# Kernel tuning notes

Measured on AMD Instinct MI355X. Metric: run time of the kernel, lower is better.

## Reference

```python
import jax, jax.numpy as jnp
import numpy as np

B, C, H, W, K = 4, 32, 64, 64, 64
BH, BW = 2, 2  # block_size
RF_THRESH = 0.05  # gaussian support threshold (lattice kernels are ~0 outside RF)


def _gaussian_lattice(key, n_kernels, h, w):
    """Build Gaussian receptive-field kernels like lattice.gaussian_kernel_lattice:
    rfs[k,i,j] = exp(-((i-mu_y)^2 + (j-mu_x)^2) / (2*sigma^2)), thresholded to
    zero outside the RF so each kernel has compact support."""
    k1, k2 = jax.random.split(key)
    mu = jax.random.uniform(k1, (n_kernels, 2), minval=8.0, maxval=h - 8.0)
    sigma = jax.random.uniform(k2, (n_kernels, 1), minval=4.0, maxval=7.0)
    yy = jnp.arange(h, dtype=jnp.float32)[:, None]
    xx = jnp.arange(w, dtype=jnp.float32)[None, :]
    d2 = (yy[None] - mu[:, 0, None, None]) ** 2 + (xx[None] - mu[:, 1, None, None]) ** 2
    g = jnp.exp(-d2 / (2.0 * sigma[:, :, None] ** 2))  # (K, h, w)
    return jnp.where(g > RF_THRESH, g, 0.0).astype(jnp.float32)


def setup_inputs() -> dict:
    key = jax.random.key(0)
    ku, kr = jax.random.split(key)
    u = jax.random.normal(ku, (B, C, H, W), dtype=jnp.float32)
    rfs = _gaussian_lattice(kr, K, H, W)
    return {"u": u, "rfs": rfs}


def reference(u, rfs):
    """RF_Pool.__call__ with pool_type='prob', block_size=(2,2): returns p_mean.

    For each receptive field k, the kernel is elementwise-multiplied with u and
    a probabilistic max-pool (Lee et al.) with an 'off' state is computed over
    the RF support:  h_mean_k = exp(u*rf_k) / (1 + sum_{RF_k} exp(u*rf_k)).
    Detection probabilities are accumulated over RFs, then pooling-unit means
    p_mean are taken as the block-wise max over block_size blocks."""
    dt = u.dtype
    mask = rfs > 0  # (K, H, W) RF supports
    neg = jnp.asarray(-1e30, dt)
    # kernel-weighted pre-activations per RF: (B, C, K, H, W)
    v = u[:, :, None, :, :] * rfs[None, None]
    vm = jnp.where(mask[None, None], v, neg)
    # stable normalization including the off-state exp(0)=1
    m = jnp.maximum(jnp.max(vm, axis=(-2, -1), keepdims=True), 0.0)
    e = jnp.where(mask[None, None], jnp.exp(v - m), 0.0)
    denom = jnp.exp(-m) + jnp.sum(e, axis=(-2, -1), keepdims=True)
    h_mean = jnp.sum(e / denom, axis=2)  # (B, C, H, W) sum over RFs
    # block-wise pooling to p_mean: (B, C, H//BH, W//BW)
    p_mean = h_mean.reshape(B, C, H // BH, BH, W // BW, BW).max(axis=(3, 5))
    return p_mean
```

## Files before the change

### kernel.cpp

```cpp
#include <hip/hip_runtime.h>
#include <hip/hip_bf16.h>

#define BB 4
#define CC 32
#define HH 64
#define WW 64
#define KK 64
#define PIX (HH * WW)
#define NBC (BB * CC)


__global__ __launch_bounds__(256) void rf_phase1(
        const float* __restrict__ u,
        const float* __restrict__ rfs,
        float* __restrict__ inv) {
    const int bc = blockIdx.x >> 4;
    const int kg = blockIdx.x & 15;
    const int t  = threadIdx.x;
    const int w  = t >> 6;
    const int l  = t & 63;

    __shared__ float su[PIX];
    {
        const float4* u4  = (const float4*)(u + (size_t)bc * PIX);
        float4*       su4 = (float4*)su;
        #pragma unroll
        for (int i = 0; i < 4; ++i) su4[t + 256 * i] = u4[t + 256 * i];
    }
    __syncthreads();

    const int k = kg * 4 + w;
    const float4* r4  = (const float4*)(rfs + (size_t)k * PIX);
    const float4* su4 = (const float4*)su;

    float s = 0.f;
    #pragma unroll
    for (int i = 0; i < 16; ++i) {
        const float4 rv = r4[64 * i + l];
        const float4 uv = su4[64 * i + l];
        const float ex = __expf(uv.x * rv.x);
        const float ey = __expf(uv.y * rv.y);
        const float ez = __expf(uv.z * rv.z);
        const float ew = __expf(uv.w * rv.w);
        s += (rv.x > 0.f) ? ex : 0.f;
        s += (rv.y > 0.f) ? ey : 0.f;
        s += (rv.z > 0.f) ? ez : 0.f;
        s += (rv.w > 0.f) ? ew : 0.f;
    }
    #pragma unroll
    for (int off = 32; off > 0; off >>= 1)
        s += __shfl_xor(s, off, 64);

    if (l == 0) inv[bc * KK + k] = 1.f / (1.f + s);
}

__global__ __launch_bounds__(256) void rf_phase2(
        const float* __restrict__ u,
        const float* __restrict__ rfs,
        const float* __restrict__ inv,
        float* __restrict__ out) {
    const int bc = blockIdx.x >> 3;
    const int rp = (blockIdx.x & 7) * 4 + (threadIdx.x >> 6);
    const int l  = threadIdx.x & 63;

    const int pbase = rp * 128 + l;
    const float u0 = u[(size_t)bc * PIX + pbase];
    const float u1 = u[(size_t)bc * PIX + pbase + 64];
    const float* __restrict__ invp = inv + bc * KK;
    const float* __restrict__ rfp  = rfs + pbase;

    float h0 = 0.f, h1 = 0.f;
    #pragma unroll 8
    for (int k = 0; k < KK; ++k) {
        const float r0 = rfp[(size_t)k * PIX];
        const float r1 = rfp[(size_t)k * PIX + 64];
        const float fi = invp[k];
        const float e0 = __expf(u0 * r0);
        const float e1 = __expf(u1 * r1);
        h0 += (r0 > 0.f) ? e0 * fi : 0.f;
        h1 += (r1 > 0.f) ? e1 * fi : 0.f;
    }

    const float v = fmaxf(h0, h1);
    const float o = fmaxf(v, __shfl_xor(v, 1, 64));
    if ((l & 1) == 0)
        out[(size_t)bc * (HH / 2) * (WW / 2) + rp * 32 + (l >> 1)] = o;
}

extern "C" void kernel_launch(void* const* d_in, const int* in_sizes, int n_in,
                              void* d_out, int out_size, void* d_ws, size_t ws_size,
                              hipStream_t stream) {
    const float* u   = (const float*)d_in[0];
    const float* rfs = (const float*)d_in[1];
    float* out       = (float*)d_out;
    float* inv       = (float*)d_ws;

    rf_phase1<<<NBC * 16, 256, 0, stream>>>(u, rfs, inv);
    rf_phase2<<<NBC * 8, 256, 0, stream>>>(u, rfs, inv, out);
}
```

Before: 73.92 us.

## Skip work outside each receptive field's bounding box via precomputed bboxes

Adds a kernel that computes the row/column bounding box of each RF's nonzero support. The normalization pass and the accumulation pass then only load and exponentiate pixels inside each RF's box, instead of scanning the full 64x64 grid for every (bc,k). Phase1 drops its shared-memory staging of u, and phase2 caches inv and bboxes in shared memory. It adds a third launch and divergent per-lane branches, but the bboxes are derived from the inputs on every call, so correctness holds for any rfs.

```diff
diff --git a/kernel.cpp b/kernel.cpp
--- a/kernel.cpp
+++ b/kernel.cpp
@@ -10,81 +10,124 @@
 #define NBC (BB * CC)
 
 
+__global__ __launch_bounds__(256) void rf_bbox(
+        const float* __restrict__ rfs, int4* __restrict__ bbox) {
+    const int k = blockIdx.x;
+    const int t = threadIdx.x;
+    const int l = t & 63;
+
+    int minr = HH, maxr = -1, minc = WW, maxc = -1;
+    const float4* r4 = (const float4*)(rfs + (size_t)k * PIX);
+    #pragma unroll
+    for (int i = 0; i < 4; ++i) {
+        const float4 v = r4[t + 256 * i];
+        const int px = 4 * (t + 256 * i);
+        const int r = px >> 6, cbase = px & 63;
+        const float vv[4] = {v.x, v.y, v.z, v.w};
+        #pragma unroll
+        for (int j = 0; j < 4; ++j) {
+            if (vv[j] > 0.f) {
+                minr = min(minr, r);       maxr = max(maxr, r);
+                minc = min(minc, cbase + j); maxc = max(maxc, cbase + j);
+            }
+        }
+    }
+    #pragma unroll
+    for (int off = 32; off > 0; off >>= 1) {
+        minr = min(minr, __shfl_xor(minr, off, 64));
+        maxr = max(maxr, __shfl_xor(maxr, off, 64));
+        minc = min(minc, __shfl_xor(minc, off, 64));
+        maxc = max(maxc, __shfl_xor(maxc, off, 64));
+    }
+    __shared__ int sb[4];
+    if (t == 0) { sb[0] = HH; sb[1] = -1; sb[2] = WW; sb[3] = -1; }
+    __syncthreads();
+    if (l == 0) {
+        atomicMin(&sb[0], minr); atomicMax(&sb[1], maxr);
+        atomicMin(&sb[2], minc); atomicMax(&sb[3], maxc);
+    }
+    __syncthreads();
+    if (t == 0) bbox[k] = make_int4(sb[0], sb[1], sb[2], sb[3]);
+}
+
 __global__ __launch_bounds__(256) void rf_phase1(
         const float* __restrict__ u,
         const float* __restrict__ rfs,
+        const int4* __restrict__ bbox,
         float* __restrict__ inv) {
-    const int bc = blockIdx.x >> 4;
-    const int kg = blockIdx.x & 15;
-    const int t  = threadIdx.x;
-    const int w  = t >> 6;
-    const int l  = t & 63;
+    const int w   = threadIdx.x >> 6;
+    const int l   = threadIdx.x & 63;
+    const int idx = blockIdx.x * 4 + w;
+    const int bc  = idx >> 6;
+    const int k   = idx & 63;
 
-    __shared__ float su[PIX];
-    {
-        const float4* u4  = (const float4*)(u + (size_t)bc * PIX);
-        float4*       su4 = (float4*)su;
-        #pragma unroll
-        for (int i = 0; i < 4; ++i) su4[t + 256 * i] = u4[t + 256 * i];
-    }
-    __syncthreads();
+    const int4 bb = bbox[k];
+    const int colbase = (l & 15) * 4;
+    const bool colact = (colbase + 3 >= bb.z) && (colbase <= bb.w);
 
-    const int k = kg * 4 + w;
-    const float4* r4  = (const float4*)(rfs + (size_t)k * PIX);
-    const float4* su4 = (const float4*)su;
+    const float* rp = rfs + (size_t)k * PIX;
+    const float* up = u + (size_t)bc * PIX;
 
     float s = 0.f;
-    #pragma unroll
-    for (int i = 0; i < 16; ++i) {
-        const float4 rv = r4[64 * i + l];
-        const float4 uv = su4[64 * i + l];
-        const float ex = __expf(uv.x * rv.x);
-        const float ey = __expf(uv.y * rv.y);
-        const float ez = __expf(uv.z * rv.z);
-        const float ew = __expf(uv.w * rv.w);
-        s += (rv.x > 0.f) ? ex : 0.f;
-        s += (rv.y > 0.f) ? ey : 0.f;
-        s += (rv.z > 0.f) ? ez : 0.f;
-        s += (rv.w > 0.f) ? ew : 0.f;
+    for (int r = bb.x + (l >> 4); r <= bb.y; r += 4) {
+        if (colact) {
+            const float4 rv = *(const float4*)(rp + r * WW + colbase);
+            const float4 uv = *(const float4*)(up + r * WW + colbase);
+            s += (rv.x > 0.f) ? __expf(uv.x * rv.x) : 0.f;
+            s += (rv.y > 0.f) ? __expf(uv.y * rv.y) : 0.f;
+            s += (rv.z > 0.f) ? __expf(uv.z * rv.z) : 0.f;
+            s += (rv.w > 0.f) ? __expf(uv.w * rv.w) : 0.f;
+        }
     }
     #pragma unroll
     for (int off = 32; off > 0; off >>= 1)
         s += __shfl_xor(s, off, 64);
-
     if (l == 0) inv[bc * KK + k] = 1.f / (1.f + s);
 }
 
 __global__ __launch_bounds__(256) void rf_phase2(
         const float* __restrict__ u,
         const float* __restrict__ rfs,
+        const int4* __restrict__ bbox,
         const float* __restrict__ inv,
         float* __restrict__ out) {
-    const int bc = blockIdx.x >> 3;
-    const int rp = (blockIdx.x & 7) * 4 + (threadIdx.x >> 6);
-    const int l  = threadIdx.x & 63;
+    const int bc    = blockIdx.x >> 3;
+    const int chunk = blockIdx.x & 7;
+    const int t     = threadIdx.x;
+    const int w     = t >> 6;
+    const int l     = t & 63;
+    const int R0    = chunk * 8 + 2 * w;
 
-    const int pbase = rp * 128 + l;
-    const float u0 = u[(size_t)bc * PIX + pbase];
-    const float u1 = u[(size_t)bc * PIX + pbase + 64];
-    const float* __restrict__ invp = inv + bc * KK;
-    const float* __restrict__ rfp  = rfs + pbase;
+    __shared__ float sinv[KK];
+    __shared__ int4  sbb[KK];
+    if (t < KK) { sinv[t] = inv[bc * KK + t]; sbb[t] = bbox[t]; }
+
+    const float u0 = u[(size_t)bc * PIX + R0 * WW + l];
+    const float u1 = u[(size_t)bc * PIX + (R0 + 1) * WW + l];
+    __syncthreads();
 
     float h0 = 0.f, h1 = 0.f;
-    #pragma unroll 8
+    #pragma unroll 4
     for (int k = 0; k < KK; ++k) {
-        const float r0 = rfp[(size_t)k * PIX];
-        const float r1 = rfp[(size_t)k * PIX + 64];
-        const float fi = invp[k];
-        const float e0 = __expf(u0 * r0);
-        const float e1 = __expf(u1 * r1);
-        h0 += (r0 > 0.f) ? e0 * fi : 0.f;
-        h1 += (r1 > 0.f) ? e1 * fi : 0.f;
+        const int4 bb = sbb[k];
+        if (bb.y < R0 || bb.x > R0 + 1) continue;
+        const float fi = sinv[k];
+        const bool colact = (l >= bb.z) && (l <= bb.w);
+        const float* rp = rfs + (size_t)k * PIX + R0 * WW + l;
+        if (colact && R0 >= bb.x && R0 <= bb.y) {
+            const float rv = rp[0];
+            h0 += (rv > 0.f) ? __expf(u0 * rv) * fi : 0.f;
+        }
+        if (colact && R0 + 1 >= bb.x && R0 + 1 <= bb.y) {
+            const float rv = rp[WW];
+            h1 += (rv > 0.f) ? __expf(u1 * rv) * fi : 0.f;
+        }
     }
 
     const float v = fmaxf(h0, h1);
     const float o = fmaxf(v, __shfl_xor(v, 1, 64));
     if ((l & 1) == 0)
-        out[(size_t)bc * (HH / 2) * (WW / 2) + rp * 32 + (l >> 1)] = o;
+        out[(size_t)bc * (HH / 2) * (WW / 2) + (chunk * 4 + w) * 32 + (l >> 1)] = o;
 }
 
 extern "C" void kernel_launch(void* const* d_in, const int* in_sizes, int n_in,
@@ -93,8 +136,10 @@
     const float* u   = (const float*)d_in[0];
     const float* rfs = (const float*)d_in[1];
     float* out       = (float*)d_out;
-    float* inv       = (float*)d_ws;
+    int4* bbox       = (int4*)d_ws;
+    float* inv       = (float*)((char*)d_ws + KK * sizeof(int4));
 
-    rf_phase1<<<NBC * 16, 256, 0, stream>>>(u, rfs, inv);
-    rf_phase2<<<NBC * 8, 256, 0, stream>>>(u, rfs, inv, out);
+    rf_bbox  <<<KK, 256, 0, stream>>>(rfs, bbox);
+    rf_phase1<<<NBC * KK / 4, 256, 0, stream>>>(u, rfs, bbox, inv);
+    rf_phase2<<<NBC * 8, 256, 0, stream>>>(u, rfs, bbox, inv, out);
 }
```

Result: slower. 88.39 us (+19.6%).

## Fuse normaliser and accumulation kernels into one block-per-image-half kernel

Applied to the files above, without the earlier changes.

Merges the two kernels into one where each block loads a (b,c) image into shared memory, computes all 64 RF normalisers into shared memory, then computes half of the pooled outputs. This removes the second launch and the global workspace round trip for the normalisers. In exchange, each normaliser set is recomputed by both halves, which adds redundant exp work, and the grid shrinks to 256 larger blocks.

```diff
diff --git a/kernel.cpp b/kernel.cpp
--- a/kernel.cpp
+++ b/kernel.cpp
@@ -10,81 +10,72 @@
 #define NBC (BB * CC)
 
 
-__global__ __launch_bounds__(256) void rf_phase1(
+__global__ __launch_bounds__(512) void rf_fused(
         const float* __restrict__ u,
         const float* __restrict__ rfs,
-        float* __restrict__ inv) {
-    const int bc = blockIdx.x >> 4;
-    const int kg = blockIdx.x & 15;
-    const int t  = threadIdx.x;
-    const int w  = t >> 6;
-    const int l  = t & 63;
+        float* __restrict__ out) {
+    const int bc   = blockIdx.x >> 1;
+    const int half = blockIdx.x & 1;
+    const int t    = threadIdx.x;
+    const int w    = t >> 6;
+    const int l    = t & 63;
 
     __shared__ float su[PIX];
+    __shared__ float sinv[KK];
+
     {
-        const float4* u4  = (const float4*)(u + (size_t)bc * PIX);
-        float4*       su4 = (float4*)su;
-        #pragma unroll
-        for (int i = 0; i < 4; ++i) su4[t + 256 * i] = u4[t + 256 * i];
+        const float4* ug = (const float4*)(u + (size_t)bc * PIX);
+        float4* s4 = (float4*)su;
+        s4[t]       = ug[t];
+        s4[t + 512] = ug[t + 512];
     }
     __syncthreads();
 
-    const int k = kg * 4 + w;
-    const float4* r4  = (const float4*)(rfs + (size_t)k * PIX);
     const float4* su4 = (const float4*)su;
 
-    float s = 0.f;
+    for (int kk = 0; kk < 8; ++kk) {
+        const int k = w * 8 + kk;
+        const float4* r4 = (const float4*)(rfs + (size_t)k * PIX);
+        float s = 0.f;
+        #pragma unroll
+        for (int i = 0; i < 16; ++i) {
+            const float4 rv = r4[i * 64 + l];
+            const float4 uv = su4[i * 64 + l];
+            s += (rv.x > 0.f) ? __expf(uv.x * rv.x) : 0.f;
+            s += (rv.y > 0.f) ? __expf(uv.y * rv.y) : 0.f;
+            s += (rv.z > 0.f) ? __expf(uv.z * rv.z) : 0.f;
+            s += (rv.w > 0.f) ? __expf(uv.w * rv.w) : 0.f;
+        }
+        #pragma unroll
+        for (int off = 32; off > 0; off >>= 1)
+            s += __shfl_xor(s, off, 64);
+        if (l == 0) sinv[k] = 1.f / (1.f + s);
+    }
+    __syncthreads();
+
     #pragma unroll
-    for (int i = 0; i < 16; ++i) {
-        const float4 rv = r4[64 * i + l];
-        const float4 uv = su4[64 * i + l];
-        const float ex = __expf(uv.x * rv.x);
-        const float ey = __expf(uv.y * rv.y);
-        const float ez = __expf(uv.z * rv.z);
-        const float ew = __expf(uv.w * rv.w);
-        s += (rv.x > 0.f) ? ex : 0.f;
-        s += (rv.y > 0.f) ? ey : 0.f;
-        s += (rv.z > 0.f) ? ez : 0.f;
-        s += (rv.w > 0.f) ? ew : 0.f;
+    for (int j = 0; j < 2; ++j) {
+        const int rp = half * 16 + w * 2 + j;
+        const int r0 = rp * 2;
+        const float u0 = su[r0 * WW + l];
+        const float u1 = su[r0 * WW + WW + l];
+        const float* rfp = rfs + r0 * WW + l;
+
+        float h0 = 0.f, h1 = 0.f;
+        #pragma unroll 8
+        for (int k = 0; k < KK; ++k) {
+            const float rv0 = rfp[(size_t)k * PIX];
+            const float rv1 = rfp[(size_t)k * PIX + WW];
+            const float fi  = sinv[k];
+            h0 += (rv0 > 0.f) ? __expf(u0 * rv0) * fi : 0.f;
+            h1 += (rv1 > 0.f) ? __expf(u1 * rv1) * fi : 0.f;
+        }
+
+        const float v = fmaxf(h0, h1);
+        const float o = fmaxf(v, __shfl_xor(v, 1, 64));
+        if ((l & 1) == 0)
+            out[(size_t)bc * (HH / 2) * (WW / 2) + rp * 32 + (l >> 1)] = o;
     }
-    #pragma unroll
-    for (int off = 32; off > 0; off >>= 1)
-        s += __shfl_xor(s, off, 64);
-
-    if (l == 0) inv[bc * KK + k] = 1.f / (1.f + s);
-}
-
-__global__ __launch_bounds__(256) void rf_phase2(
-        const float* __restrict__ u,
-        const float* __restrict__ rfs,
-        const float* __restrict__ inv,
-        float* __restrict__ out) {
-    const int bc = blockIdx.x >> 3;
-    const int rp = (blockIdx.x & 7) * 4 + (threadIdx.x >> 6);
-    const int l  = threadIdx.x & 63;
-
-    const int pbase = rp * 128 + l;
-    const float u0 = u[(size_t)bc * PIX + pbase];
-    const float u1 = u[(size_t)bc * PIX + pbase + 64];
-    const float* __restrict__ invp = inv + bc * KK;
-    const float* __restrict__ rfp  = rfs + pbase;
-
-    float h0 = 0.f, h1 = 0.f;
-    #pragma unroll 8
-    for (int k = 0; k < KK; ++k) {
-        const float r0 = rfp[(size_t)k * PIX];
-        const float r1 = rfp[(size_t)k * PIX + 64];
-        const float fi = invp[k];
-        const float e0 = __expf(u0 * r0);
-        const float e1 = __expf(u1 * r1);
-        h0 += (r0 > 0.f) ? e0 * fi : 0.f;
-        h1 += (r1 > 0.f) ? e1 * fi : 0.f;
-    }
-
-    const float v = fmaxf(h0, h1);
-    const float o = fmaxf(v, __shfl_xor(v, 1, 64));
-    if ((l & 1) == 0)
-        out[(size_t)bc * (HH / 2) * (WW / 2) + rp * 32 + (l >> 1)] = o;
 }
 
 extern "C" void kernel_launch(void* const* d_in, const int* in_sizes, int n_in,
@@ -93,8 +84,5 @@
     const float* u   = (const float*)d_in[0];
     const float* rfs = (const float*)d_in[1];
     float* out       = (float*)d_out;
-    float* inv       = (float*)d_ws;
-
-    rf_phase1<<<NBC * 16, 256, 0, stream>>>(u, rfs, inv);
-    rf_phase2<<<NBC * 8, 256, 0, stream>>>(u, rfs, inv, out);
+    rf_fused<<<NBC * 2, 512, 0, stream>>>(u, rfs, out);
 }
```

After: 112.2 us. 51.8% more time.
